# Performance work log

Measured on AMD Instinct MI355X. Metric: run time of the kernel, lower is better.

## Reference

```python
import jax, jax.numpy as jnp
import numpy as np

N = 100000   # nodes
E = 1600000  # edges
D = 128      # input_dim == hidden_dim
L = 3        # n_layers
P = 7        # n_properties
B = 64       # graphs in batch
BN_EPS = 1e-5
NEG_SLOPE = 0.2


def setup_inputs() -> dict:
    key = jax.random.key(0)
    ks = jax.random.split(key, 18)
    s = 1.0 / np.sqrt(D)
    sp = 1.0 / np.sqrt(P)
    return {
        "x": jax.random.normal(ks[0], (N, D), jnp.float32),
        "edge_index": jax.random.randint(ks[1], (2, E), 0, N, dtype=jnp.int64),
        "batch": jnp.sort(jax.random.randint(ks[2], (N,), 0, B, dtype=jnp.int64)),
        "graph_stats": jax.random.normal(ks[3], (B, P), jnp.float32),
        # GIN MLP params (stacked over layers; input_dim == hidden_dim == D)
        "W1s": jax.random.normal(ks[4], (L, D, D), jnp.float32) * s,
        "b1s": jnp.zeros((L, D), jnp.float32),
        "gammas": jnp.ones((L, D), jnp.float32),
        "betas": jnp.zeros((L, D), jnp.float32),
        "bn_means": jax.random.normal(ks[5], (L, D), jnp.float32) * 0.1,
        "bn_vars": jax.random.uniform(ks[6], (L, D), jnp.float32) + 0.5,
        "W2s": jax.random.normal(ks[7], (L, D, D), jnp.float32) * s,
        "b2s": jnp.zeros((L, D), jnp.float32),
        # stat conditioning transforms
        "statWs": jax.random.normal(ks[8], (L, P, D), jnp.float32) * sp,
        "statBs": jnp.zeros((L, D), jnp.float32),
        # fc_out
        "fcW": jax.random.normal(ks[9], (D, D), jnp.float32) * s,
        "fcB": jnp.zeros((D,), jnp.float32),
    }


def reference(x, edge_index, batch, graph_stats,
              W1s, b1s, gammas, betas, bn_means, bn_vars, W2s, b2s,
              statWs, statBs, fcW, fcB):
    # per-node graph stats (nan -> -100, then broadcast by graph id)
    node_stats = jnp.nan_to_num(graph_stats, nan=-100.0)[batch]  # [N, P]
    src, dst = edge_index[0], edge_index[1]
    h = x
    for i in range(L):
        # GIN aggregation (eps = 0): (1+eps)*h_i + sum_{j->i} h_j
        agg = jax.ops.segment_sum(h[src], dst, num_segments=N)  # [N, D]
        m = h + agg
        # MLP: Linear -> LeakyReLU(0.2) -> BatchNorm1d (eval) -> Linear -> LeakyReLU(0.2)
        m = jax.nn.leaky_relu(m @ W1s[i] + b1s[i], NEG_SLOPE)
        m = (m - bn_means[i]) * (gammas[i] / jnp.sqrt(bn_vars[i] + BN_EPS)) + betas[i]
        m = jax.nn.leaky_relu(m @ W2s[i] + b2s[i], NEG_SLOPE)
        # stats conditioning add (dropout is identity in eval mode)
        h = m + node_stats @ statWs[i] + statBs[i]
    return h @ fcW + fcB  # [N, D]
```

## Files before the change

kernel.cpp:

```cpp
#include <hip/hip_runtime.h>
#include <math.h>

#define N_NODES 100000
#define N_EDGES 1600000
#define D 128
#define L_LAYERS 3
#define P_STATS 7
#define B_GRAPHS 64
#define BN_EPS 1e-5f
#define NEG_SLOPE 0.2f

#define NB 196
#define BCAP 10240
#define EPB 6400

typedef __attribute__((ext_vector_type(8))) short bf16x8;
typedef __attribute__((ext_vector_type(4))) float f32x4;

static __device__ __forceinline__ short f2bf(float f) {
    union { float f; unsigned u; } v;
    v.f = f;
    unsigned r = v.u + 0x7fffu + ((v.u >> 16) & 1u);
    return (short)(r >> 16);
}

static __device__ __forceinline__ float bf2f(short s) {
    union { unsigned u; float f; } v;
    v.u = ((unsigned)(unsigned short)s) << 16;
    return v.f;
}


__global__ void zero_n_kernel(int* __restrict__ p, int n) {
    int i = blockIdx.x * blockDim.x + threadIdx.x;
    if (i < n) p[i] = 0;
}

__global__ __launch_bounds__(256) void bucketA_kernel(const int* __restrict__ src,
                                                      const int* __restrict__ dst,
                                                      int* __restrict__ bucket_cnt,
                                                      int2* __restrict__ bucketbuf) {
    __shared__ int s_src[EPB];
    __shared__ int s_dst[EPB];
    __shared__ int hist[NB], base[NB], loc[NB];
    const int tid = threadIdx.x;
    const int e0 = blockIdx.x * EPB;
    for (int i = tid; i < NB; i += 256) { hist[i] = 0; loc[i] = 0; }
    __syncthreads();
    for (int i = tid; i < EPB; i += 256) {
        int s = src[e0 + i];
        int d = dst[e0 + i];
        s_src[i] = s;
        s_dst[i] = d;
        atomicAdd(&hist[d >> 9], 1);
    }
    __syncthreads();
    for (int i = tid; i < NB; i += 256)
        base[i] = hist[i] ? atomicAdd(&bucket_cnt[i], hist[i]) : 0;
    __syncthreads();
    for (int i = tid; i < EPB; i += 256) {
        int d = s_dst[i];
        int b = d >> 9;
        int off = atomicAdd(&loc[b], 1);
        int idx = base[b] + off;
        if (idx < BCAP) bucketbuf[(size_t)b * BCAP + idx] = make_int2(s_src[i], d);
    }
}

__global__ __launch_bounds__(256) void bucketB1_kernel(const int* __restrict__ bucket_cnt,
                                                       const int2* __restrict__ bucketbuf,
                                                       int* __restrict__ deg) {
    __shared__ int hist[512];
    const int b = blockIdx.x;
    for (int i = threadIdx.x; i < 512; i += 256) hist[i] = 0;
    __syncthreads();
    int cnt = min(bucket_cnt[b], BCAP);
    for (int i = threadIdx.x; i < cnt; i += 256) {
        int d = bucketbuf[(size_t)b * BCAP + i].y;
        atomicAdd(&hist[d & 511], 1);
    }
    __syncthreads();
    int nbase = b << 9;
    for (int i = threadIdx.x; i < 512; i += 256) {
        int node = nbase + i;
        if (node < N_NODES) deg[node] = hist[i];
    }
}

__global__ __launch_bounds__(256) void bucketB2_kernel(const int* __restrict__ bucket_cnt,
                                                       const int2* __restrict__ bucketbuf,
                                                       int* __restrict__ cursor,
                                                       int* __restrict__ csr_src) {
    const int b = blockIdx.x;
    int cnt = min(bucket_cnt[b], BCAP);
    for (int i = threadIdx.x; i < cnt; i += 256) {
        int2 p = bucketbuf[(size_t)b * BCAP + i];
        int pos = atomicAdd(&cursor[p.y], 1);
        csr_src[pos] = p.x;
    }
}


__global__ void scan1_kernel(const int* __restrict__ deg, int* __restrict__ incl,
                             int* __restrict__ bsum) {
    __shared__ int s[256];
    const int tid = threadIdx.x;
    const int base = blockIdx.x * 2048;
    int v[8];
    int sum = 0;
    const int idx0 = base + tid * 8;
#pragma unroll
    for (int i = 0; i < 8; ++i) {
        int idx = idx0 + i;
        int d = (idx < N_NODES) ? deg[idx] : 0;
        sum += d;
        v[i] = sum;
    }
    s[tid] = sum;
    __syncthreads();
    for (int off = 1; off < 256; off <<= 1) {
        int t = (tid >= off) ? s[tid - off] : 0;
        __syncthreads();
        s[tid] += t;
        __syncthreads();
    }
    int prev = (tid > 0) ? s[tid - 1] : 0;
#pragma unroll
    for (int i = 0; i < 8; ++i) {
        int idx = idx0 + i;
        if (idx < N_NODES) incl[idx] = v[i] + prev;
    }
    if (tid == 255) bsum[blockIdx.x] = s[255];
}

__global__ void scan2_kernel(int* __restrict__ bsum, int nb) {
    if (threadIdx.x == 0 && blockIdx.x == 0) {
        int run = 0;
        for (int i = 0; i < nb; ++i) { int t = bsum[i]; bsum[i] = run; run += t; }
    }
}

__global__ void scan3_kernel(const int* __restrict__ deg, const int* __restrict__ incl,
                             const int* __restrict__ bsum, int* __restrict__ start,
                             int* __restrict__ cursor) {
    int i = blockIdx.x * blockDim.x + threadIdx.x;
    if (i < N_NODES) {
        int inc = incl[i] + bsum[i >> 11];
        int st = inc - deg[i];
        start[i] = st;
        cursor[i] = st;
    }
    if (i == 0) start[N_NODES] = N_EDGES;
}

__global__ void gproj_kernel(const float* __restrict__ gs, const float* __restrict__ statWs,
                             const float* __restrict__ statBs, float* __restrict__ gproj) {
    int b = blockIdx.x;
    int l = blockIdx.y;
    int j = threadIdx.x;
    float acc = statBs[l * D + j];
#pragma unroll
    for (int p = 0; p < P_STATS; ++p) {
        float g = gs[b * P_STATS + p];
        if (g != g) g = -100.0f;
        acc += g * statWs[(l * P_STATS + p) * D + j];
    }
    gproj[(l * B_GRAPHS + b) * D + j] = acc;
}

__global__ void wconv_kernel(const float* __restrict__ W1s, const float* __restrict__ W2s,
                             const float* __restrict__ fcW, short* __restrict__ wt) {
    int mid = blockIdx.y;
    const float* src = (mid < 3) ? (W1s + mid * D * D)
                                 : ((mid < 6) ? (W2s + (mid - 3) * D * D) : fcW);
    short* dstm = wt + mid * D * D;
    int i = blockIdx.x * 256 + threadIdx.x;
    int k = i >> 7, n = i & 127;
    dstm[n * D + k] = f2bf(src[i]);
}

__global__ __launch_bounds__(256) void xconv_kernel(const float* __restrict__ x,
                                                    short* __restrict__ xb) {
    int i = blockIdx.x * 256 + threadIdx.x;
    const float4* x4 = (const float4*)x;
    float4 a = x4[i * 2], b = x4[i * 2 + 1];
    short s[8];
    s[0] = f2bf(a.x); s[1] = f2bf(a.y); s[2] = f2bf(a.z); s[3] = f2bf(a.w);
    s[4] = f2bf(b.x); s[5] = f2bf(b.y); s[6] = f2bf(b.z); s[7] = f2bf(b.w);
    *(bf16x8*)&xb[i * 8] = *(bf16x8*)s;
}

__global__ __launch_bounds__(256) void agg_kernel(const short* __restrict__ hb,
                                                  const int* __restrict__ start,
                                                  const int* __restrict__ csr_src,
                                                  short* __restrict__ m_bf) {
    int node = blockIdx.x * 16 + (threadIdx.x >> 4);
    int c8 = threadIdx.x & 15;
    const bf16x8* h8 = (const bf16x8*)hb;

    bf16x8 own = h8[node * 16 + c8];
    float acc[8];
#pragma unroll
    for (int i = 0; i < 8; ++i) acc[i] = bf2f(own[i]);

    int s = start[node];
    int e = start[node + 1];
    int k = s;
    for (; k + 2 <= e; k += 2) {
        int sn0 = csr_src[k];
        int sn1 = csr_src[k + 1];
        bf16x8 v0 = h8[sn0 * 16 + c8];
        bf16x8 v1 = h8[sn1 * 16 + c8];
#pragma unroll
        for (int i = 0; i < 8; ++i) acc[i] += bf2f(v0[i]);
#pragma unroll
        for (int i = 0; i < 8; ++i) acc[i] += bf2f(v1[i]);
    }
    if (k < e) {
        int sn0 = csr_src[k];
        bf16x8 v0 = h8[sn0 * 16 + c8];
#pragma unroll
        for (int i = 0; i < 8; ++i) acc[i] += bf2f(v0[i]);
    }

    short pk[8];
#pragma unroll
    for (int i = 0; i < 8; ++i) pk[i] = f2bf(acc[i]);
    *(bf16x8*)&m_bf[node * D + c8 * 8] = *(bf16x8*)pk;
}

template <bool FINAL>
__global__ __launch_bounds__(256, 2) void mlp_mfma_kernel(
    const short* __restrict__ m_bf,
    const short* __restrict__ W1t,
    const float* __restrict__ b1,
    const float* __restrict__ gamma, const float* __restrict__ beta,
    const float* __restrict__ mean, const float* __restrict__ var,
    const short* __restrict__ W2t,
    const float* __restrict__ b2,
    const float* __restrict__ gproj, const int* __restrict__ batch,
    float* __restrict__ outf, short* __restrict__ outb) {
    __shared__ short sy[128 * 128];
    __shared__ float sB1[128], sSc[128], sSb[128], sB2[128];

    const int tid = threadIdx.x;
    const int wid = tid >> 6;
    const int lane = tid & 63;
    const int lr = lane & 15;
    const int lk = lane >> 4;

    if (tid < 128) {
        sB1[tid] = b1[tid];
        if (!FINAL) {
            float sc = gamma[tid] * rsqrtf(var[tid] + BN_EPS);
            sSc[tid] = sc;
            sSb[tid] = beta[tid] - mean[tid] * sc;
            sB2[tid] = b2[tid];
        }
    }
    __syncthreads();

    const int nodeBase = blockIdx.x * 128 + (wid & 1) * 64;
    const int featBase = (wid >> 1) * 64;
    const int nlBase = (wid & 1) * 64;

    int nIdx[4];
#pragma unroll
    for (int mt = 0; mt < 4; ++mt) {
        int n = nodeBase + mt * 16 + lr;
        nIdx[mt] = (n < N_NODES) ? n : (N_NODES - 1);
    }

    bf16x8 wf[4][4];
#pragma unroll
    for (int ft = 0; ft < 4; ++ft)
#pragma unroll
        for (int kt = 0; kt < 4; ++kt)
            wf[ft][kt] = *(const bf16x8*)&W1t[(featBase + ft * 16 + lr) * D + kt * 32 + lk * 8];

    f32x4 acc[4][4];
#pragma unroll
    for (int ft = 0; ft < 4; ++ft)
#pragma unroll
        for (int mt = 0; mt < 4; ++mt)
            acc[ft][mt] = (f32x4)(0.0f);

#pragma unroll
    for (int kt = 0; kt < 4; ++kt) {
        bf16x8 mf[4];
#pragma unroll
        for (int mt = 0; mt < 4; ++mt)
            mf[mt] = *(const bf16x8*)&m_bf[nIdx[mt] * D + kt * 32 + lk * 8];
#pragma unroll
        for (int ft = 0; ft < 4; ++ft)
#pragma unroll
            for (int mt = 0; mt < 4; ++mt)
                acc[ft][mt] = __builtin_amdgcn_mfma_f32_16x16x32_bf16(wf[ft][kt], mf[mt],
                                                                      acc[ft][mt], 0, 0, 0);
    }

    if (FINAL) {
#pragma unroll
        for (int mt = 0; mt < 4; ++mt) {
            int node = nodeBase + mt * 16 + lr;
            if (node < N_NODES) {
#pragma unroll
                for (int ft = 0; ft < 4; ++ft) {
                    int f0 = featBase + ft * 16 + lk * 4;
                    float4 o;
                    o.x = acc[ft][mt][0] + sB1[f0 + 0];
                    o.y = acc[ft][mt][1] + sB1[f0 + 1];
                    o.z = acc[ft][mt][2] + sB1[f0 + 2];
                    o.w = acc[ft][mt][3] + sB1[f0 + 3];
                    *(float4*)&outf[node * D + f0] = o;
                }
            }
        }
        return;
    }

#pragma unroll
    for (int ft = 0; ft < 4; ++ft) {
        int f0 = featBase + ft * 16 + lk * 4;
#pragma unroll
        for (int mt = 0; mt < 4; ++mt) {
            int nl = nlBase + mt * 16 + lr;
            short4 pk;
#pragma unroll
            for (int r = 0; r < 4; ++r) {
                float v = acc[ft][mt][r] + sB1[f0 + r];
                v = (v > 0.f) ? v : NEG_SLOPE * v;
                v = v * sSc[f0 + r] + sSb[f0 + r];
                ((short*)&pk)[r] = f2bf(v);
            }
            int byteoff = nl * 256 + f0 * 2;
            byteoff ^= (nl & 7) << 4;
            *(short4*)((char*)sy + byteoff) = pk;
        }
    }
    __syncthreads();

#pragma unroll
    for (int ft = 0; ft < 4; ++ft)
#pragma unroll
        for (int kt = 0; kt < 4; ++kt)
            wf[ft][kt] = *(const bf16x8*)&W2t[(featBase + ft * 16 + lr) * D + kt * 32 + lk * 8];

#pragma unroll
    for (int ft = 0; ft < 4; ++ft)
#pragma unroll
        for (int mt = 0; mt < 4; ++mt)
            acc[ft][mt] = (f32x4)(0.0f);

#pragma unroll
    for (int kt = 0; kt < 4; ++kt) {
        bf16x8 yf[4];
#pragma unroll
        for (int mt = 0; mt < 4; ++mt) {
            int nl = nlBase + mt * 16 + lr;
            int byteoff = nl * 256 + kt * 64 + lk * 16;
            byteoff ^= (nl & 7) << 4;
            yf[mt] = *(const bf16x8*)((char*)sy + byteoff);
        }
#pragma unroll
        for (int ft = 0; ft < 4; ++ft)
#pragma unroll
            for (int mt = 0; mt < 4; ++mt)
                acc[ft][mt] = __builtin_amdgcn_mfma_f32_16x16x32_bf16(wf[ft][kt], yf[mt],
                                                                      acc[ft][mt], 0, 0, 0);
    }

#pragma unroll
    for (int mt = 0; mt < 4; ++mt) {
        int node = nodeBase + mt * 16 + lr;
        if (node >= N_NODES) continue;
        int bid = batch[node];
#pragma unroll
        for (int ft = 0; ft < 4; ++ft) {
            int f0 = featBase + ft * 16 + lk * 4;
            const float4 gp = *(const float4*)&gproj[bid * D + f0];
            float v0 = acc[ft][mt][0] + sB2[f0 + 0]; v0 = (v0 > 0.f) ? v0 : NEG_SLOPE * v0; v0 += gp.x;
            float v1 = acc[ft][mt][1] + sB2[f0 + 1]; v1 = (v1 > 0.f) ? v1 : NEG_SLOPE * v1; v1 += gp.y;
            float v2 = acc[ft][mt][2] + sB2[f0 + 2]; v2 = (v2 > 0.f) ? v2 : NEG_SLOPE * v2; v2 += gp.z;
            float v3 = acc[ft][mt][3] + sB2[f0 + 3]; v3 = (v3 > 0.f) ? v3 : NEG_SLOPE * v3; v3 += gp.w;
            short4 pk;
            pk.x = f2bf(v0); pk.y = f2bf(v1); pk.z = f2bf(v2); pk.w = f2bf(v3);
            *(short4*)&outb[node * D + f0] = pk;
        }
    }
}


extern "C" void kernel_launch(void* const* d_in, const int* in_sizes, int n_in,
                              void* d_out, int out_size, void* d_ws, size_t ws_size,
                              hipStream_t stream) {
    const float* x = (const float*)d_in[0];
    const int* ei = (const int*)d_in[1];
    const int* src = ei;
    const int* dst = ei + N_EDGES;
    const int* batch = (const int*)d_in[2];
    const float* gs = (const float*)d_in[3];
    const float* W1s = (const float*)d_in[4];
    const float* b1s = (const float*)d_in[5];
    const float* gammas = (const float*)d_in[6];
    const float* betas = (const float*)d_in[7];
    const float* means = (const float*)d_in[8];
    const float* vars = (const float*)d_in[9];
    const float* W2s = (const float*)d_in[10];
    const float* b2s = (const float*)d_in[11];
    const float* statWs = (const float*)d_in[12];
    const float* statBs = (const float*)d_in[13];
    const float* fcW = (const float*)d_in[14];
    const float* fcB = (const float*)d_in[15];
    float* out = (float*)d_out;

    char* ws = (char*)d_ws;
    auto alloc = [&](size_t bytes) {
        char* p = ws;
        ws += (bytes + 255) / 256 * 256;
        return p;
    };
    int* deg = (int*)alloc(N_NODES * sizeof(int));
    int* incl = (int*)alloc(N_NODES * sizeof(int));
    int* bsum = (int*)alloc(64 * sizeof(int));
    int* start = (int*)alloc((N_NODES + 1) * sizeof(int));
    int* cursor = (int*)alloc(N_NODES * sizeof(int));
    int* csr_src = (int*)alloc(N_EDGES * sizeof(int));
    int* bucket_cnt = (int*)alloc(NB * sizeof(int));
    int2* bucketbuf = (int2*)alloc((size_t)NB * BCAP * sizeof(int2));
    float* gproj = (float*)alloc((size_t)L_LAYERS * B_GRAPHS * D * sizeof(float));
    short* wt = (short*)alloc((size_t)7 * D * D * sizeof(short));
    short* xb = (short*)alloc((size_t)N_NODES * D * sizeof(short));
    short* hb = (short*)alloc((size_t)N_NODES * D * sizeof(short));
    short* m_bf = (short*)alloc((size_t)N_NODES * D * sizeof(short));

    const int nscan = (N_NODES + 2047) / 2048;

    zero_n_kernel<<<1, 256, 0, stream>>>(bucket_cnt, NB);
    bucketA_kernel<<<N_EDGES / EPB, 256, 0, stream>>>(src, dst, bucket_cnt, bucketbuf);
    bucketB1_kernel<<<NB, 256, 0, stream>>>(bucket_cnt, bucketbuf, deg);
    scan1_kernel<<<nscan, 256, 0, stream>>>(deg, incl, bsum);
    scan2_kernel<<<1, 64, 0, stream>>>(bsum, nscan);
    scan3_kernel<<<(N_NODES + 255) / 256, 256, 0, stream>>>(deg, incl, bsum, start, cursor);
    bucketB2_kernel<<<NB, 256, 0, stream>>>(bucket_cnt, bucketbuf, cursor, csr_src);

    gproj_kernel<<<dim3(B_GRAPHS, L_LAYERS), D, 0, stream>>>(gs, statWs, statBs, gproj);
    wconv_kernel<<<dim3(64, 7), 256, 0, stream>>>(W1s, W2s, fcW, wt);
    xconv_kernel<<<(N_NODES * D / 8 + 255) / 256, 256, 0, stream>>>(x, xb);

    const int agg_blocks = N_NODES / 16;
    const int mlp_blocks = (N_NODES + 127) / 128;

    agg_kernel<<<agg_blocks, 256, 0, stream>>>(xb, start, csr_src, m_bf);
    mlp_mfma_kernel<false><<<mlp_blocks, 256, 0, stream>>>(
        m_bf, wt + 0 * D * D, b1s + 0 * D, gammas + 0 * D, betas + 0 * D, means + 0 * D,
        vars + 0 * D, wt + 3 * D * D, b2s + 0 * D, gproj + 0 * B_GRAPHS * D, batch, nullptr, hb);
    agg_kernel<<<agg_blocks, 256, 0, stream>>>(hb, start, csr_src, m_bf);
    mlp_mfma_kernel<false><<<mlp_blocks, 256, 0, stream>>>(
        m_bf, wt + 1 * D * D, b1s + 1 * D, gammas + 1 * D, betas + 1 * D, means + 1 * D,
        vars + 1 * D, wt + 4 * D * D, b2s + 1 * D, gproj + 1 * B_GRAPHS * D, batch, nullptr, hb);
    agg_kernel<<<agg_blocks, 256, 0, stream>>>(hb, start, csr_src, m_bf);
    mlp_mfma_kernel<false><<<mlp_blocks, 256, 0, stream>>>(
        m_bf, wt + 2 * D * D, b1s + 2 * D, gammas + 2 * D, betas + 2 * D, means + 2 * D,
        vars + 2 * D, wt + 5 * D * D, b2s + 2 * D, gproj + 2 * B_GRAPHS * D, batch, nullptr, hb);
    mlp_mfma_kernel<true><<<mlp_blocks, 256, 0, stream>>>(
        hb, wt + 6 * D * D, fcB, nullptr, nullptr, nullptr, nullptr, nullptr, nullptr, nullptr,
        batch, out, nullptr);
}
```

Before: 424.5 us.

## Fuse final fc_out GEMM into last-layer MLP kernel and unroll aggregation by four

The final fc_out GEMM now runs inside the last layer's MLP kernel. The layer output goes through swizzled LDS into a third MFMA GEMM, which removes one launch and a bf16 round trip of h through global memory. Weight fragments are now loaded per k-step instead of being held as a 4x4 register array, which lowers register pressure so non-fused instances can declare 4 waves per SIMD in launch bounds. The aggregation gather loop is unrolled to four neighbours for more memory-level parallelism. The risks are an extra LDS round trip and barrier in the fused kernel, and weight reloads on every k-step.

```diff
diff --git a/kernel.cpp b/kernel.cpp
--- a/kernel.cpp
+++ b/kernel.cpp
@@ -206,17 +206,25 @@
     int s = start[node];
     int e = start[node + 1];
     int k = s;
-    for (; k + 2 <= e; k += 2) {
+    for (; k + 4 <= e; k += 4) {
         int sn0 = csr_src[k];
         int sn1 = csr_src[k + 1];
+        int sn2 = csr_src[k + 2];
+        int sn3 = csr_src[k + 3];
         bf16x8 v0 = h8[sn0 * 16 + c8];
         bf16x8 v1 = h8[sn1 * 16 + c8];
+        bf16x8 v2 = h8[sn2 * 16 + c8];
+        bf16x8 v3 = h8[sn3 * 16 + c8];
 #pragma unroll
         for (int i = 0; i < 8; ++i) acc[i] += bf2f(v0[i]);
 #pragma unroll
         for (int i = 0; i < 8; ++i) acc[i] += bf2f(v1[i]);
-    }
-    if (k < e) {
+#pragma unroll
+        for (int i = 0; i < 8; ++i) acc[i] += bf2f(v2[i]);
+#pragma unroll
+        for (int i = 0; i < 8; ++i) acc[i] += bf2f(v3[i]);
+    }
+    for (; k < e; ++k) {
         int sn0 = csr_src[k];
         bf16x8 v0 = h8[sn0 * 16 + c8];
 #pragma unroll
@@ -229,8 +237,8 @@
     *(bf16x8*)&m_bf[node * D + c8 * 8] = *(bf16x8*)pk;
 }
 
-template <bool FINAL>
-__global__ __launch_bounds__(256, 2) void mlp_mfma_kernel(
+template <bool FUSE_FC>
+__global__ __launch_bounds__(256, FUSE_FC ? 2 : 4) void mlp_mfma_kernel(
     const short* __restrict__ m_bf,
     const short* __restrict__ W1t,
     const float* __restrict__ b1,
@@ -239,9 +247,10 @@
     const short* __restrict__ W2t,
     const float* __restrict__ b2,
     const float* __restrict__ gproj, const int* __restrict__ batch,
+    const short* __restrict__ Wft, const float* __restrict__ fcb,
     float* __restrict__ outf, short* __restrict__ outb) {
     __shared__ short sy[128 * 128];
-    __shared__ float sB1[128], sSc[128], sSb[128], sB2[128];
+    __shared__ float sB1[128], sSc[128], sSb[128], sB2[128], sFC[128];
 
     const int tid = threadIdx.x;
     const int wid = tid >> 6;
@@ -251,12 +260,11 @@
 
     if (tid < 128) {
         sB1[tid] = b1[tid];
-        if (!FINAL) {
-            float sc = gamma[tid] * rsqrtf(var[tid] + BN_EPS);
-            sSc[tid] = sc;
-            sSb[tid] = beta[tid] - mean[tid] * sc;
-            sB2[tid] = b2[tid];
-        }
+        float sc = gamma[tid] * rsqrtf(var[tid] + BN_EPS);
+        sSc[tid] = sc;
+        sSb[tid] = beta[tid] - mean[tid] * sc;
+        sB2[tid] = b2[tid];
+        if (FUSE_FC) sFC[tid] = fcb[tid];
     }
     __syncthreads();
 
@@ -271,13 +279,6 @@
         nIdx[mt] = (n < N_NODES) ? n : (N_NODES - 1);
     }
 
-    bf16x8 wf[4][4];
-#pragma unroll
-    for (int ft = 0; ft < 4; ++ft)
-#pragma unroll
-        for (int kt = 0; kt < 4; ++kt)
-            wf[ft][kt] = *(const bf16x8*)&W1t[(featBase + ft * 16 + lr) * D + kt * 32 + lk * 8];
-
     f32x4 acc[4][4];
 #pragma unroll
     for (int ft = 0; ft < 4; ++ft)
@@ -287,6 +288,10 @@
 
 #pragma unroll
     for (int kt = 0; kt < 4; ++kt) {
+        bf16x8 wfk[4];
+#pragma unroll
+        for (int ft = 0; ft < 4; ++ft)
+            wfk[ft] = *(const bf16x8*)&W1t[(featBase + ft * 16 + lr) * D + kt * 32 + lk * 8];
         bf16x8 mf[4];
 #pragma unroll
         for (int mt = 0; mt < 4; ++mt)
@@ -295,28 +300,8 @@
         for (int ft = 0; ft < 4; ++ft)
 #pragma unroll
             for (int mt = 0; mt < 4; ++mt)
-                acc[ft][mt] = __builtin_amdgcn_mfma_f32_16x16x32_bf16(wf[ft][kt], mf[mt],
+                acc[ft][mt] = __builtin_amdgcn_mfma_f32_16x16x32_bf16(wfk[ft], mf[mt],
                                                                       acc[ft][mt], 0, 0, 0);
-    }
-
-    if (FINAL) {
-#pragma unroll
-        for (int mt = 0; mt < 4; ++mt) {
-            int node = nodeBase + mt * 16 + lr;
-            if (node < N_NODES) {
-#pragma unroll
-                for (int ft = 0; ft < 4; ++ft) {
-                    int f0 = featBase + ft * 16 + lk * 4;
-                    float4 o;
-                    o.x = acc[ft][mt][0] + sB1[f0 + 0];
-                    o.y = acc[ft][mt][1] + sB1[f0 + 1];
-                    o.z = acc[ft][mt][2] + sB1[f0 + 2];
-                    o.w = acc[ft][mt][3] + sB1[f0 + 3];
-                    *(float4*)&outf[node * D + f0] = o;
-                }
-            }
-        }
-        return;
     }
 
 #pragma unroll
@@ -343,17 +328,15 @@
 #pragma unroll
     for (int ft = 0; ft < 4; ++ft)
 #pragma unroll
-        for (int kt = 0; kt < 4; ++kt)
-            wf[ft][kt] = *(const bf16x8*)&W2t[(featBase + ft * 16 + lr) * D + kt * 32 + lk * 8];
-
-#pragma unroll
-    for (int ft = 0; ft < 4; ++ft)
-#pragma unroll
         for (int mt = 0; mt < 4; ++mt)
             acc[ft][mt] = (f32x4)(0.0f);
 
 #pragma unroll
     for (int kt = 0; kt < 4; ++kt) {
+        bf16x8 wfk[4];
+#pragma unroll
+        for (int ft = 0; ft < 4; ++ft)
+            wfk[ft] = *(const bf16x8*)&W2t[(featBase + ft * 16 + lr) * D + kt * 32 + lk * 8];
         bf16x8 yf[4];
 #pragma unroll
         for (int mt = 0; mt < 4; ++mt) {
@@ -366,26 +349,95 @@
         for (int ft = 0; ft < 4; ++ft)
 #pragma unroll
             for (int mt = 0; mt < 4; ++mt)
-                acc[ft][mt] = __builtin_amdgcn_mfma_f32_16x16x32_bf16(wf[ft][kt], yf[mt],
+                acc[ft][mt] = __builtin_amdgcn_mfma_f32_16x16x32_bf16(wfk[ft], yf[mt],
                                                                       acc[ft][mt], 0, 0, 0);
     }
 
-#pragma unroll
-    for (int mt = 0; mt < 4; ++mt) {
-        int node = nodeBase + mt * 16 + lr;
-        if (node >= N_NODES) continue;
-        int bid = batch[node];
-#pragma unroll
-        for (int ft = 0; ft < 4; ++ft) {
-            int f0 = featBase + ft * 16 + lk * 4;
+    if (!FUSE_FC) {
+#pragma unroll
+        for (int mt = 0; mt < 4; ++mt) {
+            int node = nodeBase + mt * 16 + lr;
+            if (node >= N_NODES) continue;
+            int bid = batch[node];
+#pragma unroll
+            for (int ft = 0; ft < 4; ++ft) {
+                int f0 = featBase + ft * 16 + lk * 4;
+                const float4 gp = *(const float4*)&gproj[bid * D + f0];
+                float v0 = acc[ft][mt][0] + sB2[f0 + 0]; v0 = (v0 > 0.f) ? v0 : NEG_SLOPE * v0; v0 += gp.x;
+                float v1 = acc[ft][mt][1] + sB2[f0 + 1]; v1 = (v1 > 0.f) ? v1 : NEG_SLOPE * v1; v1 += gp.y;
+                float v2 = acc[ft][mt][2] + sB2[f0 + 2]; v2 = (v2 > 0.f) ? v2 : NEG_SLOPE * v2; v2 += gp.z;
+                float v3 = acc[ft][mt][3] + sB2[f0 + 3]; v3 = (v3 > 0.f) ? v3 : NEG_SLOPE * v3; v3 += gp.w;
+                short4 pk;
+                pk.x = f2bf(v0); pk.y = f2bf(v1); pk.z = f2bf(v2); pk.w = f2bf(v3);
+                *(short4*)&outb[node * D + f0] = pk;
+            }
+        }
+        return;
+    }
+
+    __syncthreads();
+#pragma unroll
+    for (int ft = 0; ft < 4; ++ft) {
+        int f0 = featBase + ft * 16 + lk * 4;
+#pragma unroll
+        for (int mt = 0; mt < 4; ++mt) {
+            int nl = nlBase + mt * 16 + lr;
+            int bid = batch[nIdx[mt]];
             const float4 gp = *(const float4*)&gproj[bid * D + f0];
+            short4 pk;
             float v0 = acc[ft][mt][0] + sB2[f0 + 0]; v0 = (v0 > 0.f) ? v0 : NEG_SLOPE * v0; v0 += gp.x;
             float v1 = acc[ft][mt][1] + sB2[f0 + 1]; v1 = (v1 > 0.f) ? v1 : NEG_SLOPE * v1; v1 += gp.y;
             float v2 = acc[ft][mt][2] + sB2[f0 + 2]; v2 = (v2 > 0.f) ? v2 : NEG_SLOPE * v2; v2 += gp.z;
             float v3 = acc[ft][mt][3] + sB2[f0 + 3]; v3 = (v3 > 0.f) ? v3 : NEG_SLOPE * v3; v3 += gp.w;
-            short4 pk;
             pk.x = f2bf(v0); pk.y = f2bf(v1); pk.z = f2bf(v2); pk.w = f2bf(v3);
-            *(short4*)&outb[node * D + f0] = pk;
+            int byteoff = nl * 256 + f0 * 2;
+            byteoff ^= (nl & 7) << 4;
+            *(short4*)((char*)sy + byteoff) = pk;
+        }
+    }
+    __syncthreads();
+
+#pragma unroll
+    for (int ft = 0; ft < 4; ++ft)
+#pragma unroll
+        for (int mt = 0; mt < 4; ++mt)
+            acc[ft][mt] = (f32x4)(0.0f);
+
+#pragma unroll
+    for (int kt = 0; kt < 4; ++kt) {
+        bf16x8 wfk[4];
+#pragma unroll
+        for (int ft = 0; ft < 4; ++ft)
+            wfk[ft] = *(const bf16x8*)&Wft[(featBase + ft * 16 + lr) * D + kt * 32 + lk * 8];
+        bf16x8 hf[4];
+#pragma unroll
+        for (int mt = 0; mt < 4; ++mt) {
+            int nl = nlBase + mt * 16 + lr;
+            int byteoff = nl * 256 + kt * 64 + lk * 16;
+            byteoff ^= (nl & 7) << 4;
+            hf[mt] = *(const bf16x8*)((char*)sy + byteoff);
+        }
+#pragma unroll
+        for (int ft = 0; ft < 4; ++ft)
+#pragma unroll
+            for (int mt = 0; mt < 4; ++mt)
+                acc[ft][mt] = __builtin_amdgcn_mfma_f32_16x16x32_bf16(wfk[ft], hf[mt],
+                                                                      acc[ft][mt], 0, 0, 0);
+    }
+
+#pragma unroll
+    for (int mt = 0; mt < 4; ++mt) {
+        int node = nodeBase + mt * 16 + lr;
+        if (node >= N_NODES) continue;
+#pragma unroll
+        for (int ft = 0; ft < 4; ++ft) {
+            int f0 = featBase + ft * 16 + lk * 4;
+            float4 o;
+            o.x = acc[ft][mt][0] + sFC[f0 + 0];
+            o.y = acc[ft][mt][1] + sFC[f0 + 1];
+            o.z = acc[ft][mt][2] + sFC[f0 + 2];
+            o.w = acc[ft][mt][3] + sFC[f0 + 3];
+            *(float4*)&outf[node * D + f0] = o;
         }
     }
 }
@@ -454,16 +506,16 @@
     agg_kernel<<<agg_blocks, 256, 0, stream>>>(xb, start, csr_src, m_bf);
     mlp_mfma_kernel<false><<<mlp_blocks, 256, 0, stream>>>(
         m_bf, wt + 0 * D * D, b1s + 0 * D, gammas + 0 * D, betas + 0 * D, means + 0 * D,
-        vars + 0 * D, wt + 3 * D * D, b2s + 0 * D, gproj + 0 * B_GRAPHS * D, batch, nullptr, hb);
+        vars + 0 * D, wt + 3 * D * D, b2s + 0 * D, gproj + 0 * B_GRAPHS * D, batch,
+        nullptr, nullptr, nullptr, hb);
     agg_kernel<<<agg_blocks, 256, 0, stream>>>(hb, start, csr_src, m_bf);
     mlp_mfma_kernel<false><<<mlp_blocks, 256, 0, stream>>>(
         m_bf, wt + 1 * D * D, b1s + 1 * D, gammas + 1 * D, betas + 1 * D, means + 1 * D,
-        vars + 1 * D, wt + 4 * D * D, b2s + 1 * D, gproj + 1 * B_GRAPHS * D, batch, nullptr, hb);
+        vars + 1 * D, wt + 4 * D * D, b2s + 1 * D, gproj + 1 * B_GRAPHS * D, batch,
+        nullptr, nullptr, nullptr, hb);
     agg_kernel<<<agg_blocks, 256, 0, stream>>>(hb, start, csr_src, m_bf);
-    mlp_mfma_kernel<false><<<mlp_blocks, 256, 0, stream>>>(
+    mlp_mfma_kernel<true><<<mlp_blocks, 256, 0, stream>>>(
         m_bf, wt + 2 * D * D, b1s + 2 * D, gammas + 2 * D, betas + 2 * D, means + 2 * D,
-        vars + 2 * D, wt + 5 * D * D, b2s + 2 * D, gproj + 2 * B_GRAPHS * D, batch, nullptr, hb);
-    mlp_mfma_kernel<true><<<mlp_blocks, 256, 0, stream>>>(
-        hb, wt + 6 * D * D, fcB, nullptr, nullptr, nullptr, nullptr, nullptr, nullptr, nullptr,
-        batch, out, nullptr);
-}
+        vars + 2 * D, wt + 5 * D * D, b2s + 2 * D, gproj + 2 * B_GRAPHS * D, batch,
+        wt + 6 * D * D, fcB, out, nullptr);
+}
```

Measured after the change: 394.1 us. -7.2%, faster.
